# Performance work log

Hardware: AMD Instinct MI355X
Metric: run time of the kernel (lower is better)

Reference implementation:

```python
import jax, jax.numpy as jnp
import numpy as np

N_COMPANY, N_INDUSTRY, E = 20000, 500, 8192
CC, CI, D, H = 256, 128, 256, 4


def setup_inputs() -> dict:
    key = jax.random.key(0)
    ks = jax.random.split(key, 14)
    p = lambda k, shape: (jax.random.normal(k, shape, jnp.float32) * 0.02)
    company_x = jax.random.normal(ks[0], (N_COMPANY, CC), jnp.float32)
    industry_x = jax.random.normal(ks[1], (N_INDUSTRY, CI), jnp.float32)
    src = jax.random.randint(ks[2], (E,), 0, N_COMPANY)
    tgt = jax.random.randint(ks[3], (E,), 0, N_INDUSTRY)
    edge_index = jnp.stack([src, tgt]).astype(jnp.int64)
    return {
        "company_x": company_x,
        "industry_x": industry_x,
        "edge_index": edge_index,
        "Wc": p(ks[4], (D, CC)), "bc": jnp.zeros((D,), jnp.float32),
        "Wi": p(ks[5], (D, CI)), "bi": jnp.zeros((D,), jnp.float32),
        "w_in": p(ks[6], (3 * D, D)), "b_in": jnp.zeros((3 * D,), jnp.float32),
        "w_out": p(ks[7], (D, D)), "b_out": jnp.zeros((D,), jnp.float32),
        "gamma": jnp.ones((D,), jnp.float32), "beta": jnp.zeros((D,), jnp.float32),
    }


def reference(company_x, industry_x, edge_index, Wc, bc, Wi, bi, w_in, b_in, w_out, b_out, gamma, beta):
    company_h = company_x @ Wc.T + bc          # [N, D]
    industry_h = industry_x @ Wi.T + bi        # [M, D]
    src, tgt = edge_index[0], edge_index[1]
    e = src.shape[0]
    d = company_h.shape[-1]
    hd = d // H

    q_in = company_h[src]                      # [E, D] gather
    kv_in = industry_h[tgt]                    # [E, D] gather

    wq, wk, wv = jnp.split(w_in, 3, axis=0)
    bq, bk, bv = jnp.split(b_in, 3)
    qh = (q_in @ wq.T + bq).reshape(e, H, hd)
    kh = (kv_in @ wk.T + bk).reshape(e, H, hd)
    vh = (kv_in @ wv.T + bv).reshape(e, H, hd)

    scale = 1.0 / jnp.sqrt(jnp.float32(hd))
    scores = jnp.einsum("qhd,khd->hqk", qh * scale, kh)   # [H, E, E]
    attn = jax.nn.softmax(scores, axis=-1)
    ctx = jnp.einsum("hqk,khd->qhd", attn, vh).reshape(e, d)
    attn_out = ctx @ w_out.T + b_out                        # [E, D]

    agg = jax.ops.segment_sum(attn_out, src, num_segments=company_h.shape[0])
    counts = jax.ops.segment_sum(jnp.ones((e,), jnp.float32), src, num_segments=company_h.shape[0])
    pooled = agg / (counts[:, None] + 1e-6)

    out = company_h + pooled
    mean = out.mean(-1, keepdims=True)
    var = out.var(-1, keepdims=True)
    return (out - mean) / jnp.sqrt(var + 1e-5) * gamma + beta
```

## Files before the change

### kernel.cpp

```cpp
#include <hip/hip_runtime.h>

#define E_EDGES 8192
#define N_COMP  20000
#define N_IND   500
#define NKEYS   512

typedef short bf16x8 __attribute__((ext_vector_type(8)));
typedef float f32x4  __attribute__((ext_vector_type(4)));

static __device__ __forceinline__ unsigned short f2bf(float v) {
    unsigned u = __builtin_bit_cast(unsigned, v);
    u = (u + 0x7FFFu + ((u >> 16) & 1u)) >> 16;
    return (unsigned short)u;
}

static __device__ __forceinline__ void cvt8(const float* __restrict__ s,
                                            unsigned short* __restrict__ d) {
    float4 a = *(const float4*)s;
    float4 b = *(const float4*)(s + 4);
    bf16x8 o;
    o[0] = (short)f2bf(a.x); o[1] = (short)f2bf(a.y);
    o[2] = (short)f2bf(a.z); o[3] = (short)f2bf(a.w);
    o[4] = (short)f2bf(b.x); o[5] = (short)f2bf(b.y);
    o[6] = (short)f2bf(b.z); o[7] = (short)f2bf(b.w);
// ... 95 lines not shown

    __shared__ char lds[48 * 1024];
    const int t = threadIdx.x, wv = t >> 6, lane = t & 63;
    const int g = lane >> 4, ln = lane & 15;
    const int sr = t >> 2, sc = (t & 3) * 8;

    if (bid < 4) {
        char* ab = lds;
        char* wb = lds + 4 * 1024;
        const int bm = bid * 64;
        f32x4 acc[16];
#pragma unroll
        for (int i = 0; i < 16; i++) acc[i] = (f32x4){0.f, 0.f, 0.f, 0.f};
        const float* aptr = w_in + (long)(bm + sr) * 256 + sc;
        for (int kc = 0; kc < 256; kc += 32) {
            __syncthreads();
            stage_f32(aptr + kc, ab, sr, sc);
#pragma unroll
            for (int p = 0; p < 4; p++) {
                int r = p * 64 + sr;
                *(bf16x8*)(wb + ((r * 64 + sc * 2) ^ SWZ(r))) =
                    *(const bf16x8*)(WcT_bf + (long)r * 256 + kc + sc);
            }
            __syncthreads();
            int ar = wv * 16 + ln;
            bf16x8 af = *(bf16x8*)(ab + ((ar * 64 + g * 16) ^ SWZ(ar)));
#pragma unroll
            for (int nj = 0; nj < 16; nj++) {
                int wr = nj * 16 + ln;
                bf16x8 bf = *(bf16x8*)(wb + ((wr * 64 + g * 16) ^ SWZ(wr)));
                acc[nj] = __builtin_amdgcn_mfma_f32_16x16x32_bf16(af, bf, acc[nj], 0, 0, 0);
            }
        }
#pragma unroll
        for (int nj = 0; nj < 16; nj++)
#pragma unroll
            for (int r = 0; r < 4; r++)
                Wcq_bf[(long)(bm + wv * 16 + g * 4 + r) * 256 + nj * 16 + ln] =
                    f2bf(acc[nj][r]);
        return;
    }

    const int rg = (bid - 4) >> 1, colh = (bid - 4) & 1;
    char* ab  = lds;
    char* wb1 = lds + 4 * 1024;
    char* ihb = lds + 16 * 1024;
    char* wb2 = lds;

    {
        f32x4 a1[16];
#pragma unroll
        for (int i = 0; i < 16; i++) a1[i] = (f32x4){0.f, 0.f, 0.f, 0.f};
        int arow = rg * 64 + sr; if (arow > N_IND - 1) arow = N_IND - 1;
        const float* aptr = industry_x + (long)arow * 128 + sc;
        for (int kc = 0; kc < 128; kc += 32) {
            __syncthreads();
            stage_f32(aptr + kc, ab, sr, sc);
#pragma unroll
            for (int p = 0; p < 4; p++) {
                int r = p * 64 + sr;
                *(bf16x8*)(wb1 + ((r * 64 + sc * 2) ^ SWZ(r))) =
                    *(const bf16x8*)(Wi_bf + (long)r * 128 + kc + sc);
            }
            __syncthreads();
            int ar = wv * 16 + ln;
            bf16x8 af = *(bf16x8*)(ab + ((ar * 64 + g * 16) ^ SWZ(ar)));
#pragma unroll
            for (int nj = 0; nj < 16; nj++) {
                int wr = nj * 16 + ln;
                bf16x8 bf = *(bf16x8*)(wb1 + ((wr * 64 + g * 16) ^ SWZ(wr)));
                a1[nj] = __builtin_amdgcn_mfma_f32_16x16x32_bf16(af, bf, a1[nj], 0, 0, 0);
            }
        }
        __syncthreads();
#pragma unroll
        for (int nj = 0; nj < 16; nj++)
#pragma unroll
            for (int r = 0; r < 4; r++) {
                int row = wv * 16 + g * 4 + r, col = nj * 16 + ln;
                *(unsigned short*)(ihb + ((row * 512 + col * 2) ^ SWZ(row))) =
                    f2bf(a1[nj][r]);
            }
    }
    __syncthreads();

    if (colh == 0) {
        f32x4 a2[16];
#pragma unroll
        for (int i = 0; i < 16; i++) a2[i] = (f32x4){0.f, 0.f, 0.f, 0.f};
        for (int kc = 0; kc < 256; kc += 32) {
            __syncthreads();
#pragma unroll
            for (int p = 0; p < 4; p++) {
                int r = p * 64 + sr;
                *(bf16x8*)(wb2 + ((r * 64 + sc * 2) ^ SWZ(r))) =
                    *(const bf16x8*)(wkv_bf + (long)r * 256 + kc + sc);
            }
            __syncthreads();
            int row = wv * 16 + ln;
            bf16x8 af = *(bf16x8*)(ihb + ((row * 512 + (kc + g * 8) * 2) ^ SWZ(row)));
#pragma unroll
            for (int nj = 0; nj < 16; nj++) {
                int wr = nj * 16 + ln;
                bf16x8 bf = *(bf16x8*)(wb2 + ((wr * 64 + g * 16) ^ SWZ(wr)));
                a2[nj] = __builtin_amdgcn_mfma_f32_16x16x32_bf16(af, bf, a2[nj], 0, 0, 0);
            }
        }
#pragma unroll
        for (int nj = 0; nj < 16; nj++)
#pragma unroll
            for (int r = 0; r < 4; r++) {
                int R = rg * 64 + wv * 16 + g * 4 + r, n = nj * 16 + ln;
                Kbuf[(long)R * 256 + n] = f2bf(a2[nj][r] + beff[256 + n]);
            }
    } else {
        const unsigned short* wp = wkv_bf + 65536;
        f32x4 a2[16];
#pragma unroll
        for (int i = 0; i < 16; i++) a2[i] = (f32x4){0.f, 0.f, 0.f, 0.f};
        for (int kc = 0; kc < 256; kc += 32) {
            __syncthreads();
#pragma unroll
            for (int p = 0; p < 4; p++) {
                int r = p * 64 + sr;
                *(bf16x8*)(wb2 + ((r * 64 + sc * 2) ^ SWZ(r))) =
                    *(const bf16x8*)(wp + (long)r * 256 + kc + sc);
            }
            __syncthreads();
#pragma unroll
            for (int mi = 0; mi < 4; mi++) {
                int arow = wv * 64 + mi * 16 + ln;
                bf16x8 af = *(bf16x8*)(wb2 + ((arow * 64 + g * 16) ^ SWZ(arow)));
#pragma unroll
                for (int t4 = 0; t4 < 4; t4++) {
                    int brow = t4 * 16 + ln;
                    bf16x8 bfr = *(bf16x8*)(ihb + ((brow * 512 + (kc + g * 8) * 2) ^ SWZ(brow)));
                    a2[mi * 4 + t4] = __builtin_amdgcn_mfma_f32_16x16x32_bf16(af, bfr, a2[mi * 4 + t4], 0, 0, 0);
                }
            }
        }
#pragma unroll
        for (int mi = 0; mi < 4; mi++)
#pragma unroll
            for (int t4 = 0; t4 < 4; t4++)
#pragma unroll
                for (int r = 0; r < 4; r++) {
                    int nrow = wv * 64 + mi * 16 + g * 4 + r;
                    VTg[(long)nrow * 512 + rg * 64 + t4 * 16 + ln] =
                        f2bf(a2[mi * 4 + t4][r] + beff[512 + nrow]);
                }
    }
}

__global__ __launch_bounds__(256, 2) void megattn(
    const float* __restrict__ company_x,
    const unsigned short* __restrict__ Wcq,
    const float* __restrict__ beff,
    const unsigned short* __restrict__ Kbuf,
    const unsigned short* __restrict__ VTg,
    const float* __restrict__ cntT,
    const unsigned short* __restrict__ wout,
    const float* __restrict__ b_out,
    const int* __restrict__ list, const int* __restrict__ nlist,
    float* __restrict__ pooled)
{
    const int M = *nlist;
    const int bm = blockIdx.x * 16;
    if (bm >= M) return;

    __shared__ char lds[32768];
    const int t = threadIdx.x, h = t >> 6, lane = t & 63;
    const int g = lane >> 4, ln = lane & 15;
    char* qbase = lds + h * 2048;
    char* xbase = lds + 8192;
    char* pbase = lds + 16384 + h * 4096;

    {
        int row = t >> 4, c0 = (t & 15) * 16;
        int mr = bm + row; if (mr > M - 1) mr = M - 1;
        const float* src = company_x + (long)list[mr] * 256 + c0;
        *(bf16x8*)(xbase + ((row * 512 + c0 * 2) ^ SWZ(row))) = cvt8r(src);
        *(bf16x8*)(xbase + ((row * 512 + c0 * 2 + 16) ^ SWZ(row))) = cvt8r(src + 8);
    }
    __syncthreads();

    bf16x8 qf0, qf1;
    {
        f32x4 qa[4];
#pragma unroll
        for (int i = 0; i < 4; i++) qa[i] = (f32x4){0.f, 0.f, 0.f, 0.f};
#pragma unroll
        for (int kc = 0; kc < 256; kc += 32) {
            bf16x8 af = *(bf16x8*)(xbase + ((ln * 512 + (kc + g * 8) * 2) ^ SWZ(ln)));
#pragma unroll
            for (int nj = 0; nj < 4; nj++) {
                bf16x8 bf = *(const bf16x8*)(Wcq + (long)(h * 64 + nj * 16 + ln) * 256 + kc + g * 8);
                qa[nj] = __builtin_amdgcn_mfma_f32_16x16x32_bf16(af, bf, qa[nj], 0, 0, 0);
            }
        }
#pragma unroll
        for (int nj = 0; nj < 4; nj++)
#pragma unroll
            for (int r = 0; r < 4; r++) {
                int row = g * 4 + r, col = nj * 16 + ln;
                *(unsigned short*)(qbase + ((row * 128 + col * 2) ^ SWZ(row))) =
                    f2bf((qa[nj][r] + beff[h * 64 + col]) * 0.125f);
            }
        qf0 = *(bf16x8*)(qbase + ((ln * 128 + g * 16) ^ SWZ(ln)));
        qf1 = *(bf16x8*)(qbase + ((ln * 128 + 64 + g * 16) ^ SWZ(ln)));
    }

    f32x4 acc[4];
#pragma unroll
    for (int i = 0; i < 4; i++) acc[i] = (f32x4){0.f, 0.f, 0.f, 0.f};
    float mreg[4] = {-1e30f, -1e30f, -1e30f, -1e30f};
    float lreg[4] = {0.f, 0.f, 0.f, 0.f};

#pragma unroll
    for (int tile = 0; tile < 2; tile++) {
        float cnt[16];
        {
            const float* cp = cntT + ln * 32 + tile * 16;
#pragma unroll
            for (int j4 = 0; j4 < 4; j4++) {
                float4 c4 = *(const float4*)(cp + j4 * 4);
                cnt[j4 * 4 + 0] = c4.x; cnt[j4 * 4 + 1] = c4.y;
                cnt[j4 * 4 + 2] = c4.z; cnt[j4 * 4 + 3] = c4.w;
            }
        }

        f32x4 S[8][2];
#pragma unroll
        for (int half = 0; half < 2; half++) {
            bf16x8 k0r[4][2], k1r[4][2];
#pragma unroll
            for (int c4 = 0; c4 < 4; c4++)
#pragma unroll
                for (int sub = 0; sub < 2; sub++) {
                    const unsigned short* kr = Kbuf +
                        (long)(tile * 256 + (half * 4 + c4) * 32 + sub * 16 + ln) * 256 + h * 64 + g * 8;
                    k0r[c4][sub] = *(const bf16x8*)(kr);
                    k1r[c4][sub] = *(const bf16x8*)(kr + 32);
                }
#pragma unroll
            for (int c4 = 0; c4 < 4; c4++)
#pragma unroll
                for (int sub = 0; sub < 2; sub++) {
                    f32x4 s = (f32x4){0.f, 0.f, 0.f, 0.f};
                    s = __builtin_amdgcn_mfma_f32_16x16x32_bf16(qf0, k0r[c4][sub], s, 0, 0, 0);
                    s = __builtin_amdgcn_mfma_f32_16x16x32_bf16(qf1, k1r[c4][sub], s, 0, 0, 0);
                    S[half * 4 + c4][sub] = s;
                }
        }

        bf16x8 vr[2][2][4];
#pragma unroll
        for (int j = 0; j < 2; j++)
#pragma unroll
            for (int t4 = 0; t4 < 4; t4++)
                vr[0][j][t4] = *(const bf16x8*)(
                    VTg + (long)(h * 64 + t4 * 16 + ln) * 512 + tile * 256 + j * 32 + g * 8);

        float tm[4] = {-1e30f, -1e30f, -1e30f, -1e30f};
#pragma unroll
        for (int c = 0; c < 8; c++)
#pragma unroll
            for (int sub = 0; sub < 2; sub++)
#pragma unroll
                for (int r = 0; r < 4; r++) tm[r] = fmaxf(tm[r], S[c][sub][r]);
#pragma unroll
        for (int st = 1; st < 16; st <<= 1)
#pragma unroll
            for (int r = 0; r < 4; r++) tm[r] = fmaxf(tm[r], __shfl_xor(tm[r], st));

        float corr[4];
#pragma unroll
        for (int r = 0; r < 4; r++) {
            float mn = fmaxf(mreg[r], tm[r]);
            corr[r] = __expf(mreg[r] - mn);
            mreg[r] = mn;
        }

        float ps[4] = {0.f, 0.f, 0.f, 0.f};
#pragma unroll
        for (int c = 0; c < 8; c++)
#pragma unroll
            for (int sub = 0; sub < 2; sub++) {
                float cv = cnt[c * 2 + sub];
#pragma unroll
                for (int r = 0; r < 4; r++) {
                    float p = cv * __expf(S[c][sub][r] - mreg[r]);
                    S[c][sub][r] = p;
                    ps[r] += p;
                }
            }
#pragma unroll
        for (int st = 1; st < 16; st <<= 1)
#pragma unroll
            for (int r = 0; r < 4; r++) ps[r] += __shfl_xor(ps[r], st);
#pragma unroll
        for (int r = 0; r < 4; r++) lreg[r] = lreg[r] * corr[r] + ps[r];
#pragma unroll
        for (int i = 0; i < 4; i++)
#pragma unroll
            for (int r = 0; r < 4; r++) acc[i][r] *= corr[r];

#pragma unroll
        for (int grp = 0; grp < 4; grp++) {
            if (grp < 3) {
#pragma unroll
                for (int j = 0; j < 2; j++)
#pragma unroll
                    for (int t4 = 0; t4 < 4; t4++)
                        vr[(grp + 1) & 1][j][t4] = *(const bf16x8*)(
                            VTg + (long)(h * 64 + t4 * 16 + ln) * 512 +
                            tile * 256 + ((grp + 1) * 2 + j) * 32 + g * 8);
            }
#pragma unroll
            for (int j = 0; j < 2; j++) {
                int c = grp * 2 + j;
                char* pb = pbase + (c & 3) * 1024;
#pragma unroll
                for (int sub = 0; sub < 2; sub++)
#pragma unroll
                    for (int r = 0; r < 4; r++) {
                        int row = g * 4 + r;
                        *(unsigned short*)(pb + ((row * 64 + (sub * 16 + ln) * 2) ^ SWZ4(row))) =
                            f2bf(S[c][sub][r]);
                    }
                bf16x8 pa = *(bf16x8*)(pb + ((ln * 64 + g * 16) ^ SWZ4(ln)));
#pragma unroll
                for (int t4 = 0; t4 < 4; t4++)
                    acc[t4] = __builtin_amdgcn_mfma_f32_16x16x32_bf16(
                        pa, vr[grp & 1][j][t4], acc[t4], 0, 0, 0);
            }
        }
    }

#pragma unroll
    for (int t4 = 0; t4 < 4; t4++)
#pragma unroll
        for (int r = 0; r < 4; r++) {
            int row = g * 4 + r, col = t4 * 16 + ln;
            *(unsigned short*)(qbase + ((row * 128 + col * 2) ^ SWZ(row))) =
                f2bf(acc[t4][r] / lreg[r]);
        }
    __syncthreads();

    {
        f32x4 oa[4];
#pragma unroll
        for (int i = 0; i < 4; i++) oa[i] = (f32x4){0.f, 0.f, 0.f, 0.f};
#pragma unroll
        for (int kc = 0; kc < 256; kc += 32) {
            int hs = kc >> 6;
            int off = (kc & 63) + g * 8;
            bf16x8 af = *(bf16x8*)(lds + hs * 2048 + ((ln * 128 + off * 2) ^ SWZ(ln)));
#pragma unroll
            for (int nj = 0; nj < 4; nj++) {
                bf16x8 bf = *(const bf16x8*)(wout + (long)(h * 64 + nj * 16 + ln) * 256 + kc + g * 8);
                oa[nj] = __builtin_amdgcn_mfma_f32_16x16x32_bf16(af, bf, oa[nj], 0, 0, 0);
            }
        }
#pragma unroll
        for (int nj = 0; nj < 4; nj++) {
            int n = h * 64 + nj * 16 + ln;
            float bv = b_out[n];
#pragma unroll
            for (int r = 0; r < 4; r++) {
                int R = bm + g * 4 + r;
                if (R < M)
                    pooled[(long)list[R] * 256 + n] = oa[nj][r] + bv;
            }
        }
    }
}

__global__ __launch_bounds__(256) void gemm_ln(
    const float* __restrict__ A, const unsigned short* __restrict__ W,
    const float* __restrict__ bias,
    const float* __restrict__ pooled, const float* __restrict__ csrc,
    const float* __restrict__ gamma, const float* __restrict__ beta,
    float* __restrict__ out, int M, int K)
{
    __shared__ unsigned short As[64 * 32];
    __shared__ unsigned short Ws[256 * 32];
    char* abase = (char*)As;
    char* wbase = (char*)Ws;

    const int bm = blockIdx.x * 64;
    const int t = threadIdx.x;
    const int wv = t >> 6, lane = t & 63, g = lane >> 4, ln = lane & 15;

    f32x4 acc[16];
#pragma unroll
    for (int i = 0; i < 16; i++) acc[i] = (f32x4){0.f, 0.f, 0.f, 0.f};

    const int sr = t >> 2;
    const int sc = (t & 3) * 8;
    int arow = bm + sr; if (arow > M - 1) arow = M - 1;
    const float* aptr = A + (long)arow * K + sc;

    for (int kc = 0; kc < K; kc += 32) {
        __syncthreads();
        stage_f32(aptr + kc, abase, sr, sc);
#pragma unroll
        for (int p = 0; p < 4; p++) {
            int r = p * 64 + sr;
            *(bf16x8*)(wbase + ((r * 64 + sc * 2) ^ SWZ(r))) =
                *(const bf16x8*)(W + (long)r * K + kc + sc);
        }
        __syncthreads();

        const int ar = wv * 16 + ln;
        bf16x8 af = *(bf16x8*)(abase + ((ar * 64 + g * 16) ^ SWZ(ar)));
#pragma unroll
        for (int nj = 0; nj < 16; nj++) {
            int wr = nj * 16 + ln;
            bf16x8 bf = *(bf16x8*)(wbase + ((wr * 64 + g * 16) ^ SWZ(wr)));
            acc[nj] = __builtin_amdgcn_mfma_f32_16x16x32_bf16(af, bf, acc[nj], 0, 0, 0);
        }
    }

#pragma unroll
    for (int r = 0; r < 4; r++) {
        int R = bm + wv * 16 + g * 4 + r;
        bool valid = R < M;
        int Rc = valid ? R : 0;
        float cntv = csrc[Rc];
        float factor = (valid && cntv > 0.f) ? cntv / (cntv + 1e-6f) : 0.f;

        float v[16];
        float sum = 0.f, sq = 0.f;
#pragma unroll
        for (int nj = 0; nj < 16; nj++) {
            int n = nj * 16 + ln;
            float x = acc[nj][r] + bias[n] + factor * pooled[(long)Rc * 256 + n];
            v[nj] = x;
            sum += x;
            sq  += x * x;
        }
#pragma unroll
        for (int st = 1; st < 16; st <<= 1) {
            sum += __shfl_xor(sum, st);
            sq  += __shfl_xor(sq,  st);
        }
        float mean = sum * (1.0f / 256.0f);
        float var  = sq * (1.0f / 256.0f) - mean * mean;
        float rstd = rsqrtf(var + 1e-5f);
        if (valid) {
#pragma unroll
            for (int nj = 0; nj < 16; nj++) {
                int n = nj * 16 + ln;
                out[(long)R * 256 + n] = (v[nj] - mean) * rstd * gamma[n] + beta[n];
            }
        }
    }
}

extern "C" void kernel_launch(void* const* d_in, const int* in_sizes, int n_in,
                              void* d_out, int out_size, void* d_ws, size_t ws_size,
                              hipStream_t stream)
{
    const float* company_x  = (const float*)d_in[0];
    const float* industry_x = (const float*)d_in[1];
    const int*   edge       = (const int*)d_in[2];
    const float* Wc         = (const float*)d_in[3];
    const float* bc         = (const float*)d_in[4];
    const float* Wi         = (const float*)d_in[5];
    const float* bi         = (const float*)d_in[6];
    const float* w_in       = (const float*)d_in[7];
    const float* b_in       = (const float*)d_in[8];
    const float* w_out      = (const float*)d_in[9];
    const float* b_out      = (const float*)d_in[10];
    const float* gamma      = (const float*)d_in[11];
    const float* beta       = (const float*)d_in[12];
    float* out = (float*)d_out;

    const int* src = edge;
    const int* tgt = edge + E_EDGES;

    float* wf = (float*)d_ws;
    size_t o = 0;
    unsigned short* Wc_bf   = (unsigned short*)(wf + o); o += 32768;
    unsigned short* wout_bf = (unsigned short*)(wf + o); o += 32768;
    unsigned short* WcT_bf  = (unsigned short*)(wf + o); o += 32768;
    unsigned short* Wi_bf   = (unsigned short*)(wf + o); o += 16384;
    unsigned short* wkv_bf  = (unsigned short*)(wf + o); o += 65536;
    unsigned short* Wcq_bf  = (unsigned short*)(wf + o); o += 32768;
    unsigned short* Kbuf    = (unsigned short*)(wf + o); o += 65536;
    unsigned short* VTg     = (unsigned short*)(wf + o); o += 65536;
    float* pooled           = wf + o; o += (size_t)N_COMP * 256;
    float* beff             = wf + o; o += 768;
    float* cntT             = wf + o; o += NKEYS;
    int*   list             = (int*)(wf + o); o += E_EDGES;
    float* csrc             = wf + o; o += N_COMP;
    float* ctgt             = wf + o; o += NKEYS;
    int*   nlist            = (int*)(wf + o); o += 4;

    hipMemsetAsync(csrc, 0, (N_COMP + NKEYS + 4) * sizeof(float), stream);

    prep<<<dim3(220), dim3(256), 0, stream>>>(
        src, tgt, Wc, Wi, w_out, w_in, bc, bi, b_in,
        csrc, ctgt, Wc_bf, wout_bf, WcT_bf, Wi_bf, wkv_bf, beff);

    fusedW<<<dim3(99), dim3(256), 0, stream>>>(
        w_in, WcT_bf, industry_x, Wi_bf, wkv_bf, beff, ctgt, csrc,
        Wcq_bf, Kbuf, VTg, cntT, list, nlist);

    megattn<<<dim3(E_EDGES / 16), dim3(256), 0, stream>>>(
        company_x, Wcq_bf, beff, Kbuf, VTg, cntT, wout_bf, b_out,
        list, nlist, pooled);

    gemm_ln<<<dim3((N_COMP + 63) / 64), dim3(256), 0, stream>>>(
        company_x, Wc_bf, bc, pooled, csrc, gamma, beta, out, N_COMP, 256);
}
```

Measured before the change: 102.6 us.

## Split attention keys across blocks and co-schedule company GEMM with attention

```diff
diff --git a/kernel.cpp b/kernel.cpp
--- a/kernel.cpp
+++ b/kernel.cpp
@@ -271,15 +271,234 @@
     }
 }
 
-__global__ __launch_bounds__(256, 2) void megattn(
+__global__ __launch_bounds__(256, 2) void attn_gemm(
     const float* __restrict__ company_x,
     const unsigned short* __restrict__ Wcq,
     const float* __restrict__ beff,
     const unsigned short* __restrict__ Kbuf,
     const unsigned short* __restrict__ VTg,
     const float* __restrict__ cntT,
-    const unsigned short* __restrict__ wout,
-    const float* __restrict__ b_out,
+    const int* __restrict__ list, const int* __restrict__ nlist,
+    const unsigned short* __restrict__ Wc_bf, const float* __restrict__ bc,
+    float* __restrict__ accP, float* __restrict__ mP, float* __restrict__ lP,
+    float* __restrict__ ch)
+{
+    __shared__ char lds[32768];
+    const int bid = blockIdx.x;
+    const int t = threadIdx.x, lane = t & 63;
+    const int g = lane >> 4, ln = lane & 15;
+
+    if (bid < 1024) {
+        const int M = *nlist;
+        const int qt = bid >> 1, ks = bid & 1;
+        const int bm = qt * 16;
+        if (bm >= M) return;
+        const int h = t >> 6;
+        char* qb    = lds + h * 2048;
+        char* xbase = lds + 8192;
+        char* pbase = lds + 16384 + h * 4096;
+
+        {
+            int row = t >> 4, c0 = (t & 15) * 16;
+            int mr = bm + row; if (mr > M - 1) mr = M - 1;
+            const float* src = company_x + (long)list[mr] * 256 + c0;
+            *(bf16x8*)(xbase + ((row * 512 + c0 * 2) ^ SWZ(row))) = cvt8r(src);
+            *(bf16x8*)(xbase + ((row * 512 + c0 * 2 + 16) ^ SWZ(row))) = cvt8r(src + 8);
+        }
+        __syncthreads();
+
+        bf16x8 qf0, qf1;
+        {
+            f32x4 qa[4];
+#pragma unroll
+            for (int i = 0; i < 4; i++) qa[i] = (f32x4){0.f, 0.f, 0.f, 0.f};
+#pragma unroll
+            for (int kc = 0; kc < 256; kc += 32) {
+                bf16x8 af = *(bf16x8*)(xbase + ((ln * 512 + (kc + g * 8) * 2) ^ SWZ(ln)));
+#pragma unroll
+                for (int nj = 0; nj < 4; nj++) {
+                    bf16x8 bf = *(const bf16x8*)(Wcq + (long)(h * 64 + nj * 16 + ln) * 256 + kc + g * 8);
+                    qa[nj] = __builtin_amdgcn_mfma_f32_16x16x32_bf16(af, bf, qa[nj], 0, 0, 0);
+                }
+            }
+#pragma unroll
+            for (int nj = 0; nj < 4; nj++)
+#pragma unroll
+                for (int r = 0; r < 4; r++) {
+                    int row = g * 4 + r, col = nj * 16 + ln;
+                    *(unsigned short*)(qb + ((row * 128 + col * 2) ^ SWZ(row))) =
+                        f2bf((qa[nj][r] + beff[h * 64 + col]) * 0.125f);
+                }
+            qf0 = *(bf16x8*)(qb + ((ln * 128 + g * 16) ^ SWZ(ln)));
+            qf1 = *(bf16x8*)(qb + ((ln * 128 + 64 + g * 16) ^ SWZ(ln)));
+        }
+
+        float cnt[16];
+        {
+            const float* cp = cntT + ln * 32 + ks * 16;
+#pragma unroll
+            for (int j4 = 0; j4 < 4; j4++) {
+                float4 c4 = *(const float4*)(cp + j4 * 4);
+                cnt[j4 * 4 + 0] = c4.x; cnt[j4 * 4 + 1] = c4.y;
+                cnt[j4 * 4 + 2] = c4.z; cnt[j4 * 4 + 3] = c4.w;
+            }
+        }
+
+        f32x4 S[8][2];
+#pragma unroll
+        for (int half = 0; half < 2; half++) {
+            bf16x8 k0r[4][2], k1r[4][2];
+#pragma unroll
+            for (int c4 = 0; c4 < 4; c4++)
+#pragma unroll
+                for (int sub = 0; sub < 2; sub++) {
+                    const unsigned short* kr = Kbuf +
+                        (long)(ks * 256 + (half * 4 + c4) * 32 + sub * 16 + ln) * 256 + h * 64 + g * 8;
+                    k0r[c4][sub] = *(const bf16x8*)(kr);
+                    k1r[c4][sub] = *(const bf16x8*)(kr + 32);
+                }
+#pragma unroll
+            for (int c4 = 0; c4 < 4; c4++)
+#pragma unroll
+                for (int sub = 0; sub < 2; sub++) {
+                    f32x4 s = (f32x4){0.f, 0.f, 0.f, 0.f};
+                    s = __builtin_amdgcn_mfma_f32_16x16x32_bf16(qf0, k0r[c4][sub], s, 0, 0, 0);
+                    s = __builtin_amdgcn_mfma_f32_16x16x32_bf16(qf1, k1r[c4][sub], s, 0, 0, 0);
+                    S[half * 4 + c4][sub] = s;
+                }
+        }
+
+        bf16x8 vr[2][4];
+#pragma unroll
+        for (int t4 = 0; t4 < 4; t4++)
+            vr[0][t4] = *(const bf16x8*)(
+                VTg + (long)(h * 64 + t4 * 16 + ln) * 512 + ks * 256 + g * 8);
+
+        float tm[4] = {-1e30f, -1e30f, -1e30f, -1e30f};
+#pragma unroll
+        for (int c = 0; c < 8; c++)
+#pragma unroll
+            for (int sub = 0; sub < 2; sub++)
+#pragma unroll
+                for (int r = 0; r < 4; r++) tm[r] = fmaxf(tm[r], S[c][sub][r]);
+#pragma unroll
+        for (int st = 1; st < 16; st <<= 1)
+#pragma unroll
+            for (int r = 0; r < 4; r++) tm[r] = fmaxf(tm[r], __shfl_xor(tm[r], st));
+
+        float ps[4] = {0.f, 0.f, 0.f, 0.f};
+#pragma unroll
+        for (int c = 0; c < 8; c++)
+#pragma unroll
+            for (int sub = 0; sub < 2; sub++) {
+                float cv = cnt[c * 2 + sub];
+#pragma unroll
+                for (int r = 0; r < 4; r++) {
+                    float p = cv * __expf(S[c][sub][r] - tm[r]);
+                    S[c][sub][r] = p;
+                    ps[r] += p;
+                }
+            }
+#pragma unroll
+        for (int st = 1; st < 16; st <<= 1)
+#pragma unroll
+            for (int r = 0; r < 4; r++) ps[r] += __shfl_xor(ps[r], st);
+
+        f32x4 acc[4];
+#pragma unroll
+        for (int i = 0; i < 4; i++) acc[i] = (f32x4){0.f, 0.f, 0.f, 0.f};
+#pragma unroll
+        for (int c = 0; c < 8; c++) {
+            if (c < 7) {
+#pragma unroll
+                for (int t4 = 0; t4 < 4; t4++)
+                    vr[(c + 1) & 1][t4] = *(const bf16x8*)(
+                        VTg + (long)(h * 64 + t4 * 16 + ln) * 512 +
+                        ks * 256 + (c + 1) * 32 + g * 8);
+            }
+            char* pb = pbase + (c & 1) * 1024;
+#pragma unroll
+            for (int sub = 0; sub < 2; sub++)
+#pragma unroll
+                for (int r = 0; r < 4; r++) {
+                    int row = g * 4 + r;
+                    *(unsigned short*)(pb + ((row * 64 + (sub * 16 + ln) * 2) ^ SWZ4(row))) =
+                        f2bf(S[c][sub][r]);
+                }
+            bf16x8 pa = *(bf16x8*)(pb + ((ln * 64 + g * 16) ^ SWZ4(ln)));
+#pragma unroll
+            for (int t4 = 0; t4 < 4; t4++)
+                acc[t4] = __builtin_amdgcn_mfma_f32_16x16x32_bf16(
+                    pa, vr[c & 1][t4], acc[t4], 0, 0, 0);
+        }
+
+#pragma unroll
+        for (int t4 = 0; t4 < 4; t4++)
+#pragma unroll
+            for (int r = 0; r < 4; r++)
+                accP[((long)ks * E_EDGES + bm + g * 4 + r) * 256 + h * 64 + t4 * 16 + ln] =
+                    acc[t4][r];
+        if (ln == 0) {
+#pragma unroll
+            for (int r = 0; r < 4; r++) {
+                mP[(ks * 4 + h) * E_EDGES + bm + g * 4 + r] = tm[r];
+                lP[(ks * 4 + h) * E_EDGES + bm + g * 4 + r] = ps[r];
+            }
+        }
+        return;
+    }
+
+    {
+        const int bm = (bid - 1024) * 64;
+        char* abase = lds;
+        char* wbase = lds + 4096;
+        const int wv = t >> 6;
+        const int sr = t >> 2, sc = (t & 3) * 8;
+
+        f32x4 acc[16];
+#pragma unroll
+        for (int i = 0; i < 16; i++) acc[i] = (f32x4){0.f, 0.f, 0.f, 0.f};
+
+        int arow = bm + sr; if (arow > N_COMP - 1) arow = N_COMP - 1;
+        const float* aptr = company_x + (long)arow * 256 + sc;
+
+        for (int kc = 0; kc < 256; kc += 32) {
+            __syncthreads();
+            stage_f32(aptr + kc, abase, sr, sc);
+#pragma unroll
+            for (int p = 0; p < 4; p++) {
+                int r = p * 64 + sr;
+                *(bf16x8*)(wbase + ((r * 64 + sc * 2) ^ SWZ(r))) =
+                    *(const bf16x8*)(Wc_bf + (long)r * 256 + kc + sc);
+            }
+            __syncthreads();
+            const int ar = wv * 16 + ln;
+            bf16x8 af = *(bf16x8*)(abase + ((ar * 64 + g * 16) ^ SWZ(ar)));
+#pragma unroll
+            for (int nj = 0; nj < 16; nj++) {
+                int wr = nj * 16 + ln;
+                bf16x8 bf = *(bf16x8*)(wbase + ((wr * 64 + g * 16) ^ SWZ(wr)));
+                acc[nj] = __builtin_amdgcn_mfma_f32_16x16x32_bf16(af, bf, acc[nj], 0, 0, 0);
+            }
+        }
+#pragma unroll
+        for (int nj = 0; nj < 16; nj++) {
+            int n = nj * 16 + ln;
+            float bv = bc[n];
+#pragma unroll
+            for (int r = 0; r < 4; r++) {
+                int m = bm + wv * 16 + g * 4 + r;
+                if (m < N_COMP)
+                    ch[(long)m * 256 + n] = acc[nj][r] + bv;
+            }
+        }
+    }
+}
+
+__global__ __launch_bounds__(256, 2) void merge_out(
+    const float* __restrict__ accP, const float* __restrict__ mP,
+    const float* __restrict__ lP,
+    const unsigned short* __restrict__ wout, const float* __restrict__ b_out,
     const int* __restrict__ list, const int* __restrict__ nlist,
     float* __restrict__ pooled)
 {
@@ -287,294 +506,108 @@
     const int bm = blockIdx.x * 16;
     if (bm >= M) return;
 
-    __shared__ char lds[32768];
+    __shared__ char lds[8192];
     const int t = threadIdx.x, h = t >> 6, lane = t & 63;
     const int g = lane >> 4, ln = lane & 15;
-    char* qbase = lds + h * 2048;
-    char* xbase = lds + 8192;
-    char* pbase = lds + 16384 + h * 4096;
-
-    {
-        int row = t >> 4, c0 = (t & 15) * 16;
-        int mr = bm + row; if (mr > M - 1) mr = M - 1;
-        const float* src = company_x + (long)list[mr] * 256 + c0;
-        *(bf16x8*)(xbase + ((row * 512 + c0 * 2) ^ SWZ(row))) = cvt8r(src);
-        *(bf16x8*)(xbase + ((row * 512 + c0 * 2 + 16) ^ SWZ(row))) = cvt8r(src + 8);
-    }
+    char* qb = lds + h * 2048;
+
+    float s0[4], s1[4];
+    int gr[4];
+#pragma unroll
+    for (int r = 0; r < 4; r++) {
+        int R = bm + g * 4 + r;
+        gr[r] = (R > M - 1) ? (M - 1) : R;
+        float m0 = mP[(0 + h) * E_EDGES + gr[r]];
+        float m1 = mP[(4 + h) * E_EDGES + gr[r]];
+        float l0 = lP[(0 + h) * E_EDGES + gr[r]];
+        float l1 = lP[(4 + h) * E_EDGES + gr[r]];
+        float mn = fmaxf(m0, m1);
+        float c0 = __expf(m0 - mn), c1 = __expf(m1 - mn);
+        float inv = 1.0f / (l0 * c0 + l1 * c1);
+        s0[r] = c0 * inv;
+        s1[r] = c1 * inv;
+    }
+#pragma unroll
+    for (int t4 = 0; t4 < 4; t4++)
+#pragma unroll
+        for (int r = 0; r < 4; r++) {
+            int col = h * 64 + t4 * 16 + ln;
+            float a0 = accP[((long)0 * E_EDGES + gr[r]) * 256 + col];
+            float a1 = accP[((long)1 * E_EDGES + gr[r]) * 256 + col];
+            float ctx = a0 * s0[r] + a1 * s1[r];
+            int row = g * 4 + r, c2 = t4 * 16 + ln;
+            *(unsigned short*)(qb + ((row * 128 + c2 * 2) ^ SWZ(row))) = f2bf(ctx);
+        }
     __syncthreads();
 
-    bf16x8 qf0, qf1;
-    {
-        f32x4 qa[4];
-#pragma unroll
-        for (int i = 0; i < 4; i++) qa[i] = (f32x4){0.f, 0.f, 0.f, 0.f};
-#pragma unroll
-        for (int kc = 0; kc < 256; kc += 32) {
-            bf16x8 af = *(bf16x8*)(xbase + ((ln * 512 + (kc + g * 8) * 2) ^ SWZ(ln)));
-#pragma unroll
-            for (int nj = 0; nj < 4; nj++) {
-                bf16x8 bf = *(const bf16x8*)(Wcq + (long)(h * 64 + nj * 16 + ln) * 256 + kc + g * 8);
-                qa[nj] = __builtin_amdgcn_mfma_f32_16x16x32_bf16(af, bf, qa[nj], 0, 0, 0);
-            }
-        }
-#pragma unroll
-        for (int nj = 0; nj < 4; nj++)
-#pragma unroll
-            for (int r = 0; r < 4; r++) {
-                int row = g * 4 + r, col = nj * 16 + ln;
-                *(unsigned short*)(qbase + ((row * 128 + col * 2) ^ SWZ(row))) =
-                    f2bf((qa[nj][r] + beff[h * 64 + col]) * 0.125f);
-            }
-        qf0 = *(bf16x8*)(qbase + ((ln * 128 + g * 16) ^ SWZ(ln)));
-        qf1 = *(bf16x8*)(qbase + ((ln * 128 + 64 + g * 16) ^ SWZ(ln)));
-    }
-
-    f32x4 acc[4];
-#pragma unroll
-    for (int i = 0; i < 4; i++) acc[i] = (f32x4){0.f, 0.f, 0.f, 0.f};
-    float mreg[4] = {-1e30f, -1e30f, -1e30f, -1e30f};
-    float lreg[4] = {0.f, 0.f, 0.f, 0.f};
-
-#pragma unroll
-    for (int tile = 0; tile < 2; tile++) {
-        float cnt[16];
-        {
-            const float* cp = cntT + ln * 32 + tile * 16;
-#pragma unroll
-            for (int j4 = 0; j4 < 4; j4++) {
-                float4 c4 = *(const float4*)(cp + j4 * 4);
-                cnt[j4 * 4 + 0] = c4.x; cnt[j4 * 4 + 1] = c4.y;
-                cnt[j4 * 4 + 2] = c4.z; cnt[j4 * 4 + 3] = c4.w;
-            }
-        }
-
-        f32x4 S[8][2];
-#pragma unroll
-        for (int half = 0; half < 2; half++) {
-            bf16x8 k0r[4][2], k1r[4][2];
-#pragma unroll
-            for (int c4 = 0; c4 < 4; c4++)
-#pragma unroll
-                for (int sub = 0; sub < 2; sub++) {
-                    const unsigned short* kr = Kbuf +
-                        (long)(tile * 256 + (half * 4 + c4) * 32 + sub * 16 + ln) * 256 + h * 64 + g * 8;
-                    k0r[c4][sub] = *(const bf16x8*)(kr);
-                    k1r[c4][sub] = *(const bf16x8*)(kr + 32);
-                }
-#pragma unroll
-            for (int c4 = 0; c4 < 4; c4++)
-#pragma unroll
-                for (int sub = 0; sub < 2; sub++) {
-                    f32x4 s = (f32x4){0.f, 0.f, 0.f, 0.f};
-                    s = __builtin_amdgcn_mfma_f32_16x16x32_bf16(qf0, k0r[c4][sub], s, 0, 0, 0);
-                    s = __builtin_amdgcn_mfma_f32_16x16x32_bf16(qf1, k1r[c4][sub], s, 0, 0, 0);
-                    S[half * 4 + c4][sub] = s;
-                }
-        }
-
-        bf16x8 vr[2][2][4];
-#pragma unroll
-        for (int j = 0; j < 2; j++)
-#pragma unroll
-            for (int t4 = 0; t4 < 4; t4++)
-                vr[0][j][t4] = *(const bf16x8*)(
-                    VTg + (long)(h * 64 + t4 * 16 + ln) * 512 + tile * 256 + j * 32 + g * 8);
-
-        float tm[4] = {-1e30f, -1e30f, -1e30f, -1e30f};
-#pragma unroll
-        for (int c = 0; c < 8; c++)
-#pragma unroll
-            for (int sub = 0; sub < 2; sub++)
-#pragma unroll
-                for (int r = 0; r < 4; r++) tm[r] = fmaxf(tm[r], S[c][sub][r]);
-#pragma unroll
-        for (int st = 1; st < 16; st <<= 1)
-#pragma unroll
-            for (int r = 0; r < 4; r++) tm[r] = fmaxf(tm[r], __shfl_xor(tm[r], st));
-
-        float corr[4];
+    f32x4 oa[4];
+#pragma unroll
+    for (int i = 0; i < 4; i++) oa[i] = (f32x4){0.f, 0.f, 0.f, 0.f};
+#pragma unroll
+    for (int kc = 0; kc < 256; kc += 32) {
+        int hs = kc >> 6;
+        int off = (kc & 63) + g * 8;
+        bf16x8 af = *(bf16x8*)(lds + hs * 2048 + ((ln * 128 + off * 2) ^ SWZ(ln)));
+#pragma unroll
+        for (int nj = 0; nj < 4; nj++) {
+            bf16x8 bf = *(const bf16x8*)(wout + (long)(h * 64 + nj * 16 + ln) * 256 + kc + g * 8);
+            oa[nj] = __builtin_amdgcn_mfma_f32_16x16x32_bf16(af, bf, oa[nj], 0, 0, 0);
+        }
+    }
+#pragma unroll
+    for (int nj = 0; nj < 4; nj++) {
+        int n = h * 64 + nj * 16 + ln;
+        float bv = b_out[n];
 #pragma unroll
         for (int r = 0; r < 4; r++) {
-            float mn = fmaxf(mreg[r], tm[r]);
-            corr[r] = __expf(mreg[r] - mn);
-            mreg[r] = mn;
-        }
-
-        float ps[4] = {0.f, 0.f, 0.f, 0.f};
-#pragma unroll
-        for (int c = 0; c < 8; c++)
-#pragma unroll
-            for (int sub = 0; sub < 2; sub++) {
-                float cv = cnt[c * 2 + sub];
-#pragma unroll
-                for (int r = 0; r < 4; r++) {
-                    float p = cv * __expf(S[c][sub][r] - mreg[r]);
-                    S[c][sub][r] = p;
-                    ps[r] += p;
-                }
-            }
-#pragma unroll
-        for (int st = 1; st < 16; st <<= 1)
-#pragma unroll
-            for (int r = 0; r < 4; r++) ps[r] += __shfl_xor(ps[r], st);
-#pragma unroll
-        for (int r = 0; r < 4; r++) lreg[r] = lreg[r] * corr[r] + ps[r];
-#pragma unroll
-        for (int i = 0; i < 4; i++)
-#pragma unroll
-            for (int r = 0; r < 4; r++) acc[i][r] *= corr[r];
-
-#pragma unroll
-        for (int grp = 0; grp < 4; grp++) {
-            if (grp < 3) {
-#pragma unroll
-                for (int j = 0; j < 2; j++)
-#pragma unroll
-                    for (int t4 = 0; t4 < 4; t4++)
-                        vr[(grp + 1) & 1][j][t4] = *(const bf16x8*)(
-                            VTg + (long)(h * 64 + t4 * 16 + ln) * 512 +
-                            tile * 256 + ((grp + 1) * 2 + j) * 32 + g * 8);
-            }
-#pragma unroll
-            for (int j = 0; j < 2; j++) {
-                int c = grp * 2 + j;
-                char* pb = pbase + (c & 3) * 1024;
-#pragma unroll
-                for (int sub = 0; sub < 2; sub++)
-#pragma unroll
-                    for (int r = 0; r < 4; r++) {
-                        int row = g * 4 + r;
-                        *(unsigned short*)(pb + ((row * 64 + (sub * 16 + ln) * 2) ^ SWZ4(row))) =
-                            f2bf(S[c][sub][r]);
-                    }
-                bf16x8 pa = *(bf16x8*)(pb + ((ln * 64 + g * 16) ^ SWZ4(ln)));
-#pragma unroll
-                for (int t4 = 0; t4 < 4; t4++)
-                    acc[t4] = __builtin_amdgcn_mfma_f32_16x16x32_bf16(
-                        pa, vr[grp & 1][j][t4], acc[t4], 0, 0, 0);
-            }
-        }
-    }
-
-#pragma unroll
-    for (int t4 = 0; t4 < 4; t4++)
-#pragma unroll
-        for (int r = 0; r < 4; r++) {
-            int row = g * 4 + r, col = t4 * 16 + ln;
-            *(unsigned short*)(qbase + ((row * 128 + col * 2) ^ SWZ(row))) =
-                f2bf(acc[t4][r] / lreg[r]);
-        }
-    __syncthreads();
-
-    {
-        f32x4 oa[4];
-#pragma unroll
-        for (int i = 0; i < 4; i++) oa[i] = (f32x4){0.f, 0.f, 0.f, 0.f};
-#pragma unroll
-        for (int kc = 0; kc < 256; kc += 32) {
-            int hs = kc >> 6;
-            int off = (kc & 63) + g * 8;
-            bf16x8 af = *(bf16x8*)(lds + hs * 2048 + ((ln * 128 + off * 2) ^ SWZ(ln)));
-#pragma unroll
-            for (int nj = 0; nj < 4; nj++) {
-                bf16x8 bf = *(const bf16x8*)(wout + (long)(h * 64 + nj * 16 + ln) * 256 + kc + g * 8);
-                oa[nj] = __builtin_amdgcn_mfma_f32_16x16x32_bf16(af, bf, oa[nj], 0, 0, 0);
-            }
-        }
-#pragma unroll
-        for (int nj = 0; nj < 4; nj++) {
-            int n = h * 64 + nj * 16 + ln;
-            float bv = b_out[n];
-#pragma unroll
-            for (int r = 0; r < 4; r++) {
-                int R = bm + g * 4 + r;
-                if (R < M)
-                    pooled[(long)list[R] * 256 + n] = oa[nj][r] + bv;
-            }
-        }
-    }
-}
-
-__global__ __launch_bounds__(256) void gemm_ln(
-    const float* __restrict__ A, const unsigned short* __restrict__ W,
-    const float* __restrict__ bias,
-    const float* __restrict__ pooled, const float* __restrict__ csrc,
-    const float* __restrict__ gamma, const float* __restrict__ beta,
-    float* __restrict__ out, int M, int K)
+            int R = bm + g * 4 + r;
+            if (R < M)
+                pooled[(long)list[R] * 256 + n] = oa[nj][r] + bv;
+        }
+    }
+}
+
+__global__ __launch_bounds__(256) void fuse_ln(
+    const float* __restrict__ ch, const float* __restrict__ pooled,
+    const float* __restrict__ csrc, const float* __restrict__ gamma,
+    const float* __restrict__ beta, float* __restrict__ out)
 {
-    __shared__ unsigned short As[64 * 32];
-    __shared__ unsigned short Ws[256 * 32];
-    char* abase = (char*)As;
-    char* wbase = (char*)Ws;
-
-    const int bm = blockIdx.x * 64;
-    const int t = threadIdx.x;
-    const int wv = t >> 6, lane = t & 63, g = lane >> 4, ln = lane & 15;
-
-    f32x4 acc[16];
-#pragma unroll
-    for (int i = 0; i < 16; i++) acc[i] = (f32x4){0.f, 0.f, 0.f, 0.f};
-
-    const int sr = t >> 2;
-    const int sc = (t & 3) * 8;
-    int arow = bm + sr; if (arow > M - 1) arow = M - 1;
-    const float* aptr = A + (long)arow * K + sc;
-
-    for (int kc = 0; kc < K; kc += 32) {
-        __syncthreads();
-        stage_f32(aptr + kc, abase, sr, sc);
-#pragma unroll
-        for (int p = 0; p < 4; p++) {
-            int r = p * 64 + sr;
-            *(bf16x8*)(wbase + ((r * 64 + sc * 2) ^ SWZ(r))) =
-                *(const bf16x8*)(W + (long)r * K + kc + sc);
-        }
-        __syncthreads();
-
-        const int ar = wv * 16 + ln;
-        bf16x8 af = *(bf16x8*)(abase + ((ar * 64 + g * 16) ^ SWZ(ar)));
-#pragma unroll
-        for (int nj = 0; nj < 16; nj++) {
-            int wr = nj * 16 + ln;
-            bf16x8 bf = *(bf16x8*)(wbase + ((wr * 64 + g * 16) ^ SWZ(wr)));
-            acc[nj] = __builtin_amdgcn_mfma_f32_16x16x32_bf16(af, bf, acc[nj], 0, 0, 0);
-        }
-    }
-
-#pragma unroll
-    for (int r = 0; r < 4; r++) {
-        int R = bm + wv * 16 + g * 4 + r;
-        bool valid = R < M;
-        int Rc = valid ? R : 0;
-        float cntv = csrc[Rc];
-        float factor = (valid && cntv > 0.f) ? cntv / (cntv + 1e-6f) : 0.f;
-
-        float v[16];
-        float sum = 0.f, sq = 0.f;
-#pragma unroll
-        for (int nj = 0; nj < 16; nj++) {
-            int n = nj * 16 + ln;
-            float x = acc[nj][r] + bias[n] + factor * pooled[(long)Rc * 256 + n];
-            v[nj] = x;
-            sum += x;
-            sq  += x * x;
-        }
-#pragma unroll
-        for (int st = 1; st < 16; st <<= 1) {
-            sum += __shfl_xor(sum, st);
-            sq  += __shfl_xor(sq,  st);
-        }
-        float mean = sum * (1.0f / 256.0f);
-        float var  = sq * (1.0f / 256.0f) - mean * mean;
-        float rstd = rsqrtf(var + 1e-5f);
-        if (valid) {
-#pragma unroll
-            for (int nj = 0; nj < 16; nj++) {
-                int n = nj * 16 + ln;
-                out[(long)R * 256 + n] = (v[nj] - mean) * rstd * gamma[n] + beta[n];
-            }
-        }
-    }
+    const int w = threadIdx.x >> 6, lane = threadIdx.x & 63;
+    const int r = blockIdx.x * 4 + w;
+
+    const float4 c = *(const float4*)&ch[(long)r * 256 + lane * 4];
+    const float cnt = csrc[r];
+    float4 ag = {0.f, 0.f, 0.f, 0.f};
+    float factor = 0.f;
+    if (cnt > 0.f) {
+        ag = *(const float4*)&pooled[(long)r * 256 + lane * 4];
+        factor = cnt / (cnt + 1e-6f);
+    }
+
+    float o0 = c.x + ag.x * factor;
+    float o1 = c.y + ag.y * factor;
+    float o2 = c.z + ag.z * factor;
+    float o3 = c.w + ag.w * factor;
+
+    float sum = o0 + o1 + o2 + o3;
+    float sq  = o0 * o0 + o1 * o1 + o2 * o2 + o3 * o3;
+#pragma unroll
+    for (int off = 1; off < 64; off <<= 1) {
+        sum += __shfl_xor(sum, off);
+        sq  += __shfl_xor(sq,  off);
+    }
+    const float mean = sum * (1.0f / 256.0f);
+    const float var  = sq * (1.0f / 256.0f) - mean * mean;
+    const float rstd = rsqrtf(var + 1e-5f);
+
+    const float4 gm = *(const float4*)&gamma[lane * 4];
+    const float4 bt = *(const float4*)&beta[lane * 4];
+    float4 o;
+    o.x = (o0 - mean) * rstd * gm.x + bt.x;
+    o.y = (o1 - mean) * rstd * gm.y + bt.y;
+    o.z = (o2 - mean) * rstd * gm.z + bt.z;
+    o.w = (o3 - mean) * rstd * gm.w + bt.w;
+    *(float4*)&out[(long)r * 256 + lane * 4] = o;
 }
 
 extern "C" void kernel_launch(void* const* d_in, const int* in_sizes, int n_in,
@@ -609,7 +642,11 @@
     unsigned short* Wcq_bf  = (unsigned short*)(wf + o); o += 32768;
     unsigned short* Kbuf    = (unsigned short*)(wf + o); o += 65536;
     unsigned short* VTg     = (unsigned short*)(wf + o); o += 65536;
+    float* ch               = wf + o; o += (size_t)N_COMP * 256;
     float* pooled           = wf + o; o += (size_t)N_COMP * 256;
+    float* accP             = wf + o; o += (size_t)2 * E_EDGES * 256;
+    float* mPb              = wf + o; o += (size_t)8 * E_EDGES;
+    float* lPb              = wf + o; o += (size_t)8 * E_EDGES;
     float* beff             = wf + o; o += 768;
     float* cntT             = wf + o; o += NKEYS;
     int*   list             = (int*)(wf + o); o += E_EDGES;
@@ -627,10 +664,13 @@
         w_in, WcT_bf, industry_x, Wi_bf, wkv_bf, beff, ctgt, csrc,
         Wcq_bf, Kbuf, VTg, cntT, list, nlist);
 
-    megattn<<<dim3(E_EDGES / 16), dim3(256), 0, stream>>>(
-        company_x, Wcq_bf, beff, Kbuf, VTg, cntT, wout_bf, b_out,
-        list, nlist, pooled);
-
-    gemm_ln<<<dim3((N_COMP + 63) / 64), dim3(256), 0, stream>>>(
-        company_x, Wc_bf, bc, pooled, csrc, gamma, beta, out, N_COMP, 256);
-}
+    attn_gemm<<<dim3(1024 + 313), dim3(256), 0, stream>>>(
+        company_x, Wcq_bf, beff, Kbuf, VTg, cntT, list, nlist,
+        Wc_bf, bc, accP, mPb, lPb, ch);
+
+    merge_out<<<dim3(512), dim3(256), 0, stream>>>(
+        accP, mPb, lPb, wout_bf, b_out, list, nlist, pooled);
+
+    fuse_ln<<<dim3(N_COMP / 4), dim3(256), 0, stream>>>(
+        ch, pooled, csrc, gamma, beta, out);
+}
```

After: 112.5 us. 9.6% more time.

## Split Q projection into own kernel and fuse out-projection into GEMM+LayerNorm

Applied to the files above, without the earlier changes.

```diff
diff --git a/kernel.cpp b/kernel.cpp
--- a/kernel.cpp
+++ b/kernel.cpp
@@ -271,62 +271,87 @@
     }
 }
 
-__global__ __launch_bounds__(256, 2) void megattn(
-    const float* __restrict__ company_x,
-    const unsigned short* __restrict__ Wcq,
-    const float* __restrict__ beff,
+__global__ __launch_bounds__(256) void qproj(
+    const float* __restrict__ company_x, const int* __restrict__ list,
+    const int* __restrict__ nlist, const unsigned short* __restrict__ Wcq,
+    const float* __restrict__ beff, unsigned short* __restrict__ Qb)
+{
+    const int M = *nlist;
+    const int bm = blockIdx.x * 64;
+    if (bm >= M) return;
+
+    __shared__ unsigned short As[64 * 32];
+    __shared__ unsigned short Ws[256 * 32];
+    char* abase = (char*)As;
+    char* wbase = (char*)Ws;
+
+    const int t = threadIdx.x;
+    const int wv = t >> 6, lane = t & 63, g = lane >> 4, ln = lane & 15;
+
+    f32x4 acc[16];
+#pragma unroll
+    for (int i = 0; i < 16; i++) acc[i] = (f32x4){0.f, 0.f, 0.f, 0.f};
+
+    const int sr = t >> 2;
+    const int sc = (t & 3) * 8;
+    int mrow = bm + sr; if (mrow > M - 1) mrow = M - 1;
+    const float* aptr = company_x + (long)list[mrow] * 256 + sc;
+
+    for (int kc = 0; kc < 256; kc += 32) {
+        __syncthreads();
+        stage_f32(aptr + kc, abase, sr, sc);
+#pragma unroll
+        for (int p = 0; p < 4; p++) {
+            int r = p * 64 + sr;
+            *(bf16x8*)(wbase + ((r * 64 + sc * 2) ^ SWZ(r))) =
+                *(const bf16x8*)(Wcq + (long)r * 256 + kc + sc);
+        }
+        __syncthreads();
+        const int ar = wv * 16 + ln;
+        bf16x8 af = *(bf16x8*)(abase + ((ar * 64 + g * 16) ^ SWZ(ar)));
+#pragma unroll
+        for (int nj = 0; nj < 16; nj++) {
+            int wr = nj * 16 + ln;
+            bf16x8 bf = *(bf16x8*)(wbase + ((wr * 64 + g * 16) ^ SWZ(wr)));
+            acc[nj] = __builtin_amdgcn_mfma_f32_16x16x32_bf16(af, bf, acc[nj], 0, 0, 0);
+        }
+    }
+#pragma unroll
+    for (int nj = 0; nj < 16; nj++) {
+        int n = nj * 16 + ln;
+        float bv = beff[n];
+#pragma unroll
+        for (int r = 0; r < 4; r++) {
+            int m = bm + wv * 16 + g * 4 + r;
+            if (m < M)
+                Qb[(long)m * 256 + n] = f2bf((acc[nj][r] + bv) * 0.125f);
+        }
+    }
+}
+
+__global__ __launch_bounds__(256) void megattn(
+    const unsigned short* __restrict__ Qb,
     const unsigned short* __restrict__ Kbuf,
     const unsigned short* __restrict__ VTg,
     const float* __restrict__ cntT,
-    const unsigned short* __restrict__ wout,
-    const float* __restrict__ b_out,
     const int* __restrict__ list, const int* __restrict__ nlist,
-    float* __restrict__ pooled)
+    unsigned short* __restrict__ ctx_sc)
 {
     const int M = *nlist;
     const int bm = blockIdx.x * 16;
     if (bm >= M) return;
 
-    __shared__ char lds[32768];
+    __shared__ char lds[16384];
     const int t = threadIdx.x, h = t >> 6, lane = t & 63;
     const int g = lane >> 4, ln = lane & 15;
-    char* qbase = lds + h * 2048;
-    char* xbase = lds + 8192;
-    char* pbase = lds + 16384 + h * 4096;
-
-    {
-        int row = t >> 4, c0 = (t & 15) * 16;
-        int mr = bm + row; if (mr > M - 1) mr = M - 1;
-        const float* src = company_x + (long)list[mr] * 256 + c0;
-        *(bf16x8*)(xbase + ((row * 512 + c0 * 2) ^ SWZ(row))) = cvt8r(src);
-        *(bf16x8*)(xbase + ((row * 512 + c0 * 2 + 16) ^ SWZ(row))) = cvt8r(src + 8);
-    }
-    __syncthreads();
+    char* pbase = lds + h * 4096;
 
     bf16x8 qf0, qf1;
     {
-        f32x4 qa[4];
-#pragma unroll
-        for (int i = 0; i < 4; i++) qa[i] = (f32x4){0.f, 0.f, 0.f, 0.f};
-#pragma unroll
-        for (int kc = 0; kc < 256; kc += 32) {
-            bf16x8 af = *(bf16x8*)(xbase + ((ln * 512 + (kc + g * 8) * 2) ^ SWZ(ln)));
-#pragma unroll
-            for (int nj = 0; nj < 4; nj++) {
-                bf16x8 bf = *(const bf16x8*)(Wcq + (long)(h * 64 + nj * 16 + ln) * 256 + kc + g * 8);
-                qa[nj] = __builtin_amdgcn_mfma_f32_16x16x32_bf16(af, bf, qa[nj], 0, 0, 0);
-            }
-        }
-#pragma unroll
-        for (int nj = 0; nj < 4; nj++)
-#pragma unroll
-            for (int r = 0; r < 4; r++) {
-                int row = g * 4 + r, col = nj * 16 + ln;
-                *(unsigned short*)(qbase + ((row * 128 + col * 2) ^ SWZ(row))) =
-                    f2bf((qa[nj][r] + beff[h * 64 + col]) * 0.125f);
-            }
-        qf0 = *(bf16x8*)(qbase + ((ln * 128 + g * 16) ^ SWZ(ln)));
-        qf1 = *(bf16x8*)(qbase + ((ln * 128 + 64 + g * 16) ^ SWZ(ln)));
+        int qrow = bm + ln; if (qrow > M - 1) qrow = M - 1;
+        const unsigned short* qp = Qb + (long)qrow * 256 + h * 64 + g * 8;
+        qf0 = *(const bf16x8*)(qp);
+        qf1 = *(const bf16x8*)(qp + 32);
     }
 
     f32x4 acc[4];
@@ -457,87 +482,75 @@
     }
 
 #pragma unroll
-    for (int t4 = 0; t4 < 4; t4++)
-#pragma unroll
-        for (int r = 0; r < 4; r++) {
-            int row = g * 4 + r, col = t4 * 16 + ln;
-            *(unsigned short*)(qbase + ((row * 128 + col * 2) ^ SWZ(row))) =
-                f2bf(acc[t4][r] / lreg[r]);
-        }
-    __syncthreads();
-
-    {
-        f32x4 oa[4];
-#pragma unroll
-        for (int i = 0; i < 4; i++) oa[i] = (f32x4){0.f, 0.f, 0.f, 0.f};
-#pragma unroll
-        for (int kc = 0; kc < 256; kc += 32) {
-            int hs = kc >> 6;
-            int off = (kc & 63) + g * 8;
-            bf16x8 af = *(bf16x8*)(lds + hs * 2048 + ((ln * 128 + off * 2) ^ SWZ(ln)));
-#pragma unroll
-            for (int nj = 0; nj < 4; nj++) {
-                bf16x8 bf = *(const bf16x8*)(wout + (long)(h * 64 + nj * 16 + ln) * 256 + kc + g * 8);
-                oa[nj] = __builtin_amdgcn_mfma_f32_16x16x32_bf16(af, bf, oa[nj], 0, 0, 0);
-            }
-        }
-#pragma unroll
-        for (int nj = 0; nj < 4; nj++) {
-            int n = h * 64 + nj * 16 + ln;
-            float bv = b_out[n];
-#pragma unroll
-            for (int r = 0; r < 4; r++) {
-                int R = bm + g * 4 + r;
-                if (R < M)
-                    pooled[(long)list[R] * 256 + n] = oa[nj][r] + bv;
-            }
+    for (int r = 0; r < 4; r++) {
+        int R = bm + g * 4 + r;
+        if (R < M) {
+            long base = (long)list[R] * 256 + h * 64;
+#pragma unroll
+            for (int t4 = 0; t4 < 4; t4++)
+                ctx_sc[base + t4 * 16 + ln] = f2bf(acc[t4][r] / lreg[r]);
         }
     }
 }
 
 __global__ __launch_bounds__(256) void gemm_ln(
-    const float* __restrict__ A, const unsigned short* __restrict__ W,
-    const float* __restrict__ bias,
-    const float* __restrict__ pooled, const float* __restrict__ csrc,
-    const float* __restrict__ gamma, const float* __restrict__ beta,
-    float* __restrict__ out, int M, int K)
+    const float* __restrict__ A, const unsigned short* __restrict__ ctx_sc,
+    const unsigned short* __restrict__ W, const float* __restrict__ bias,
+    const unsigned short* __restrict__ wout, const float* __restrict__ b_out,
+    const float* __restrict__ csrc, const float* __restrict__ gamma,
+    const float* __restrict__ beta, float* __restrict__ out, int M)
 {
     __shared__ unsigned short As[64 * 32];
+    __shared__ unsigned short Cs[64 * 32];
     __shared__ unsigned short Ws[256 * 32];
+    __shared__ unsigned short Os[256 * 32];
     char* abase = (char*)As;
+    char* cbase = (char*)Cs;
     char* wbase = (char*)Ws;
+    char* obase = (char*)Os;
 
     const int bm = blockIdx.x * 64;
     const int t = threadIdx.x;
     const int wv = t >> 6, lane = t & 63, g = lane >> 4, ln = lane & 15;
 
-    f32x4 acc[16];
-#pragma unroll
-    for (int i = 0; i < 16; i++) acc[i] = (f32x4){0.f, 0.f, 0.f, 0.f};
+    f32x4 acc[16], oacc[16];
+#pragma unroll
+    for (int i = 0; i < 16; i++) {
+        acc[i]  = (f32x4){0.f, 0.f, 0.f, 0.f};
+        oacc[i] = (f32x4){0.f, 0.f, 0.f, 0.f};
+    }
 
     const int sr = t >> 2;
     const int sc = (t & 3) * 8;
     int arow = bm + sr; if (arow > M - 1) arow = M - 1;
-    const float* aptr = A + (long)arow * K + sc;
-
-    for (int kc = 0; kc < K; kc += 32) {
+    const float* aptr = A + (long)arow * 256 + sc;
+    const unsigned short* cptr = ctx_sc + (long)arow * 256 + sc;
+
+    for (int kc = 0; kc < 256; kc += 32) {
         __syncthreads();
         stage_f32(aptr + kc, abase, sr, sc);
+        *(bf16x8*)(cbase + ((sr * 64 + sc * 2) ^ SWZ(sr))) =
+            *(const bf16x8*)(cptr + kc);
 #pragma unroll
         for (int p = 0; p < 4; p++) {
             int r = p * 64 + sr;
             *(bf16x8*)(wbase + ((r * 64 + sc * 2) ^ SWZ(r))) =
-                *(const bf16x8*)(W + (long)r * K + kc + sc);
+                *(const bf16x8*)(W + (long)r * 256 + kc + sc);
+            *(bf16x8*)(obase + ((r * 64 + sc * 2) ^ SWZ(r))) =
+                *(const bf16x8*)(wout + (long)r * 256 + kc + sc);
         }
         __syncthreads();
 
         const int ar = wv * 16 + ln;
         bf16x8 af = *(bf16x8*)(abase + ((ar * 64 + g * 16) ^ SWZ(ar)));
+        bf16x8 cf = *(bf16x8*)(cbase + ((ar * 64 + g * 16) ^ SWZ(ar)));
 #pragma unroll
         for (int nj = 0; nj < 16; nj++) {
             int wr = nj * 16 + ln;
             bf16x8 bf = *(bf16x8*)(wbase + ((wr * 64 + g * 16) ^ SWZ(wr)));
-            acc[nj] = __builtin_amdgcn_mfma_f32_16x16x32_bf16(af, bf, acc[nj], 0, 0, 0);
+            bf16x8 of = *(bf16x8*)(obase + ((wr * 64 + g * 16) ^ SWZ(wr)));
+            acc[nj]  = __builtin_amdgcn_mfma_f32_16x16x32_bf16(af, bf, acc[nj], 0, 0, 0);
+            oacc[nj] = __builtin_amdgcn_mfma_f32_16x16x32_bf16(cf, of, oacc[nj], 0, 0, 0);
         }
     }
 
@@ -554,7 +567,7 @@
 #pragma unroll
         for (int nj = 0; nj < 16; nj++) {
             int n = nj * 16 + ln;
-            float x = acc[nj][r] + bias[n] + factor * pooled[(long)Rc * 256 + n];
+            float x = acc[nj][r] + bias[n] + factor * (oacc[nj][r] + b_out[n]);
             v[nj] = x;
             sum += x;
             sq  += x * x;
@@ -609,7 +622,8 @@
     unsigned short* Wcq_bf  = (unsigned short*)(wf + o); o += 32768;
     unsigned short* Kbuf    = (unsigned short*)(wf + o); o += 65536;
     unsigned short* VTg     = (unsigned short*)(wf + o); o += 65536;
-    float* pooled           = wf + o; o += (size_t)N_COMP * 256;
+    unsigned short* Qb      = (unsigned short*)(wf + o); o += (size_t)E_EDGES * 128;
+    unsigned short* ctx_sc  = (unsigned short*)(wf + o); o += (size_t)N_COMP * 128;
     float* beff             = wf + o; o += 768;
     float* cntT             = wf + o; o += NKEYS;
     int*   list             = (int*)(wf + o); o += E_EDGES;
@@ -627,10 +641,13 @@
         w_in, WcT_bf, industry_x, Wi_bf, wkv_bf, beff, ctgt, csrc,
         Wcq_bf, Kbuf, VTg, cntT, list, nlist);
 
-    megattn<<<dim3(E_EDGES / 16), dim3(256), 0, stream>>>(
-        company_x, Wcq_bf, beff, Kbuf, VTg, cntT, wout_bf, b_out,
-        list, nlist, pooled);
+    qproj<<<dim3(128), dim3(256), 0, stream>>>(
+        company_x, list, nlist, Wcq_bf, beff, Qb);
+
+    megattn<<<dim3(512), dim3(256), 0, stream>>>(
+        Qb, Kbuf, VTg, cntT, list, nlist, ctx_sc);
 
     gemm_ln<<<dim3((N_COMP + 63) / 64), dim3(256), 0, stream>>>(
-        company_x, Wc_bf, bc, pooled, csrc, gamma, beta, out, N_COMP, 256);
-}
+        company_x, ctx_sc, Wc_bf, bc, wout_bf, b_out,
+        csrc, gamma, beta, out, N_COMP);
+}
```

Result: slower. 112.2 us (+9.4%).
